# Performance work log

Measured on AMD Instinct MI355X. Metric: run time of the kernel, lower is better.

Reference implementation:

```python
import jax, jax.numpy as jnp
import numpy as np

B, T, H, LAT, ADIM = 8192, 40, 100, 10, 2
ATT_TEMP = 5.0


def setup_inputs() -> dict:
    key = jax.random.key(0)
    ks = jax.random.split(key, 12)
    return {
        "sampled_att_z": jax.random.normal(ks[0], (B, LAT), jnp.float32),
        "enc_h": jax.random.normal(ks[1], (B, H), jnp.float32),
        # keep IDM params strictly positive / physically plausible to avoid inf
        "idm_params": 1.0 + 2.0 * jax.random.uniform(ks[2], (B, 5), jnp.float32),
        "idm_s": jax.random.uniform(ks[3], (B, T, 8), jnp.float32),
        "sdv_acts": jax.random.normal(ks[4], (B, T, ADIM), jnp.float32),
        "linear_W": jax.random.normal(ks[5], (LAT, H), jnp.float32) / np.float32(np.sqrt(LAT)),
        "linear_b": jnp.zeros((H,), jnp.float32),
        "lstm_Wx": jax.random.normal(ks[6], (H + ADIM, 4 * H), jnp.float32) / np.float32(np.sqrt(H + ADIM)),
        "lstm_Wh": jax.random.normal(ks[7], (H, 4 * H), jnp.float32) / np.float32(np.sqrt(H)),
        "lstm_b": jnp.zeros((4 * H,), jnp.float32),
        "att_W": jax.random.normal(ks[8], (H, 1), jnp.float32) / np.float32(np.sqrt(H)),
        "att_b": jnp.zeros((1,), jnp.float32),
        # precomputed per-step noise, replacing tf.random.normal inside the loop
        "noise_f": jax.random.normal(ks[9], (T, B, 1), jnp.float32),
        "noise_m": jax.random.normal(ks[10], (T, B, 1), jnp.float32),
    }


def reference(sampled_att_z, enc_h, idm_params, idm_s, sdv_acts,
              linear_W, linear_b, lstm_Wx, lstm_Wh, lstm_b, att_W, att_b,
              noise_f, noise_m):
    desired_v = idm_params[:, 0:1]
    desired_tgap = idm_params[:, 1:2]
    min_jamx = idm_params[:, 2:3]
    max_act = idm_params[:, 3:4]
    min_act = idm_params[:, 4:5]

    def idm_driver(vel, dv, dx):  # all [B,1]
        dx = jnp.clip(dx, 0.5, 1000.0)
        desired_gap = min_jamx + jax.nn.relu(
            desired_tgap * vel + vel * dv / (2.0 * jnp.sqrt(max_act * min_act)))
        act = max_act * (1.0 - (vel / desired_v) ** 4 - (desired_gap / dx) ** 2)
        return jnp.clip(act, -3.0, 3.0)

    att_proj = sampled_att_z @ linear_W + linear_b  # [B,H]; also the att_context and init h,c

    s_tm = jnp.swapaxes(idm_s, 0, 1)      # [T,B,8]
    a_tm = jnp.swapaxes(sdv_acts, 0, 1)   # [T,B,ADIM]

    ego_v0 = idm_s[:, 0, 0:1]
    ego_x0 = idm_s[:, 0, 3:4]
    zero_act = jnp.zeros_like(ego_v0)  # step-0 kinematic update is a no-op

    def step(carry, xs):
        ego_v, ego_x, h, c, act = carry
        s, sdv, nf, nm = xs
        ego_v = ego_v + act * 0.1
        ego_x = ego_x + ego_v * 0.1 + 0.5 * act * 0.1 ** 2

        f_v, m_v = s[:, 1:2], s[:, 2:3]
        f_x, m_x = s[:, 4:5], s[:, 5:6]
        f_ex, m_ex = s[:, 6:7], s[:, 7:8]

        ef_act = idm_driver(ego_v, ego_v - f_v, f_x - ego_x)
        ef_act = f_ex * ef_act + (1.0 - f_ex) * nf
        em_act = idm_driver(ego_v, ego_v - m_v, m_x - ego_x)
        em_act = m_ex * em_act + (1.0 - m_ex) * nm

        x_in = jnp.concatenate([att_proj, sdv], axis=-1)  # [B,H+ADIM]
        z = x_in @ lstm_Wx + h @ lstm_Wh + lstm_b          # [B,4H], keras gate order i,f,g,o
        zi, zf, zg, zo = jnp.split(z, 4, axis=-1)
        c = jax.nn.sigmoid(zf) * c + jax.nn.sigmoid(zi) * jnp.tanh(zg)
        h = jax.nn.sigmoid(zo) * jnp.tanh(c)

        att_score = jax.nn.sigmoid(ATT_TEMP * (h @ att_W + att_b))  # [B,1]
        act = (1.0 - att_score) * ef_act + att_score * em_act
        return (ego_v, ego_x, h, c, act), (act, att_score)

    init = (ego_v0, ego_x0, att_proj, att_proj, zero_act)
    _, (acts, atts) = jax.lax.scan(step, init, (s_tm, a_tm, noise_f, noise_m))
    act_seq = jnp.swapaxes(acts, 0, 1)  # [B,T,1]
    att_seq = jnp.swapaxes(atts, 0, 1)  # [B,T,1]
    return act_seq, att_seq
```

## Files before the change

### kernel.cpp

```cpp
#include <hip/hip_runtime.h>
#include <math.h>


#define B_TOT 8192
#define T_STEPS 40
#define NB 16

typedef _Float16 f16;
typedef f16 f16x8 __attribute__((ext_vector_type(8)));
typedef float f32x4 __attribute__((ext_vector_type(4)));

__device__ __forceinline__ float rcpf(float x) { return __builtin_amdgcn_rcpf(x); }
__device__ __forceinline__ float ex2(float x)  { return __builtin_amdgcn_exp2f(x); }
__device__ __forceinline__ float sigf(float x)  { return rcpf(1.f + ex2(-1.44269504f * x)); }
__device__ __forceinline__ float tanhf_(float x){ return fmaf(-2.f, rcpf(1.f + ex2(2.88539008f * x)), 1.f); }


__global__ __launch_bounds__(256) void idm_prep(
    const float* __restrict__ Wx, const float* __restrict__ Wh,
    const float* __restrict__ bvec, const float* __restrict__ attw,
    f16* __restrict__ whb, f16* __restrict__ wxb,
    float* __restrict__ bp)
{
  int i = blockIdx.x * 256 + threadIdx.x;
  int k = i >> 9, n = i & 511;
  int g = n >> 7, j128 = n & 127;
  float vh = 0.f, vx = 0.f;
  if (j128 < 100) {
    int col = g * 100 + j128;
    if (k < 100)      { vh = Wh[k * 400 + col]; vx = Wx[k * 400 + col]; }
    else if (k < 102) { vh = Wx[k * 400 + col]; }
  } else if (n == 100 && k < 100) {
    vh = attw[k];
  }
  int idx = (((n >> 4) * 4 + (k >> 5)) * 64 + (((k >> 3) & 3) * 16 + (n & 15))) * 8 + (k & 7);
  whb[idx] = (f16)vh;
  wxb[idx] = (f16)vx;
  if (i < 512) { int gg = i >> 7, jj = i & 127; bp[i] = (jj < 100) ? bvec[gg * 100 + jj] : 0.f; }
}

__global__ __launch_bounds__(448, 4) void idm_main(
    const float* __restrict__ z_att,
    const float* __restrict__ linear_W,
    const float* __restrict__ linear_b,
    const float* __restrict__ sdv_acts,
    const f16* __restrict__ whb, const f16* __restrict__ wxb,
    const float* __restrict__ bp,
    const float* __restrict__ idm_params,
    const float* __restrict__ idm_s,
    const float* __restrict__ att_b,
    const float* __restrict__ noise_f,
    const float* __restrict__ noise_m,
    float* __restrict__ out)
{
  __shared__ f16   hS[2][16][136];
  __shared__ f16   sdvS[T_STEPS][16][2];
  __shared__ float logitS[T_STEPS][16];
  __shared__ float sS[16][T_STEPS][6];
  __shared__ float nS[2][T_STEPS][16];
  __shared__ float accS[2][16][T_STEPS];

  const int tid = threadIdx.x;
  const int w  = tid >> 6;
  const int l  = tid & 63;
  const int lr = l & 15;
  const int lq = l >> 4;
  const int b0g = blockIdx.x * NB;
  const int jcol = 16 * w + lr;

  for (int idx = tid; idx < 2176; idx += 448) ((unsigned*)hS)[idx] = 0u;
  for (int idx = tid; idx < 1280; idx += 448) {
    float v = sdv_acts[(size_t)b0g * 80 + idx];
    int b = idx / 80, r = idx - b * 80;
    sdvS[r >> 1][b][r & 1] = (f16)v;
  }
  for (int idx = tid; idx < 5120; idx += 448) {
    int f = idx & 7;
    if (f != 0 && f != 3) {
      int b = idx / 320, rem = idx - b * 320, t = rem >> 3;
      sS[b][t][(f < 3) ? f - 1 : f - 2] = idm_s[(size_t)b0g * 320 + idx];
    }
  }
  for (int idx = tid; idx < 1280; idx += 448) {
    int which = idx >= 640 ? 1 : 0;
    int r = idx - which * 640;
    int t = r >> 4, i = r & 15;
    nS[which][t][i] = which ? noise_m[(size_t)t * B_TOT + b0g + i]
                            : noise_f[(size_t)t * B_TOT + b0g + i];
  }
  __syncthreads();

  if (tid < 256) {
    int b = tid >> 4, oct = tid & 15;
    float za[10];
    #pragma unroll
    for (int t2 = 0; t2 < 10; ++t2) za[t2] = z_att[(b0g + b) * 10 + t2];
    #pragma unroll
    for (int jj = 0; jj < 8; ++jj) {
      int j = oct * 8 + jj;
      if (j < 100) {
        float acc = linear_b[j];
        #pragma unroll
        for (int t2 = 0; t2 < 10; ++t2) acc = fmaf(za[t2], linear_W[t2 * 100 + j], acc);
        hS[0][b][j] = (f16)acc;
      }
    }
  }
  if (tid < 32) hS[0][tid >> 1][100 + (tid & 1)] = sdvS[0][tid >> 1][tid & 1];
  __syncthreads();

  f16x8 wb[4][4];
  #pragma unroll
  for (int g = 0; g < 4; ++g) {
    int tile = w + 8 * g;
    #pragma unroll
    for (int kf = 0; kf < 4; ++kf)
      wb[g][kf] = *(const f16x8*)(wxb + ((size_t)(tile * 4 + kf) * 64 + l) * 8);
  }
  f32x4 cx[4];
  #pragma unroll
  for (int g = 0; g < 4; ++g) {
    float bpv = bp[(w + 8 * g) * 16 + lr];
    f32x4 c = {bpv, bpv, bpv, bpv};
    cx[g] = c;
  }
  #pragma unroll
  for (int kf = 0; kf < 4; ++kf) {
    f16x8 a = *(const f16x8*)(&hS[0][lr][kf * 32 + lq * 8]);
    #pragma unroll
    for (int g = 0; g < 4; ++g)
      cx[g] = __builtin_amdgcn_mfma_f32_16x16x32_f16(a, wb[g][kf], cx[g], 0, 0, 0);
  }
  #pragma unroll
  for (int g = 0; g < 4; ++g) {
    int tile = w + 8 * g;
    #pragma unroll
    for (int kf = 0; kf < 4; ++kf)
      wb[g][kf] = *(const f16x8*)(whb + ((size_t)(tile * 4 + kf) * 64 + l) * 8);
  }

  float cst[4];
  #pragma unroll
  for (int r = 0; r < 4; ++r) cst[r] = (float)hS[0][lq * 4 + r][jcol];

  int p = 0;
  for (int t = 0; t < T_STEPS; ++t) {
    f16x8 a0 = *(const f16x8*)(&hS[p][lr][0  + lq * 8]);
    f16x8 a1 = *(const f16x8*)(&hS[p][lr][32 + lq * 8]);
    f16x8 a2 = *(const f16x8*)(&hS[p][lr][64 + lq * 8]);
    f16x8 a3 = *(const f16x8*)(&hS[p][lr][96 + lq * 8]);
    f32x4 z0 = cx[0], z1 = cx[1], z2 = cx[2], z3 = cx[3];
    z0 = __builtin_amdgcn_mfma_f32_16x16x32_f16(a0, wb[0][0], z0, 0, 0, 0);
    z1 = __builtin_amdgcn_mfma_f32_16x16x32_f16(a0, wb[1][0], z1, 0, 0, 0);
    z2 = __builtin_amdgcn_mfma_f32_16x16x32_f16(a0, wb[2][0], z2, 0, 0, 0);
    z3 = __builtin_amdgcn_mfma_f32_16x16x32_f16(a0, wb[3][0], z3, 0, 0, 0);
    z0 = __builtin_amdgcn_mfma_f32_16x16x32_f16(a1, wb[0][1], z0, 0, 0, 0);
    z1 = __builtin_amdgcn_mfma_f32_16x16x32_f16(a1, wb[1][1], z1, 0, 0, 0);
    z2 = __builtin_amdgcn_mfma_f32_16x16x32_f16(a1, wb[2][1], z2, 0, 0, 0);
    z3 = __builtin_amdgcn_mfma_f32_16x16x32_f16(a1, wb[3][1], z3, 0, 0, 0);
    z0 = __builtin_amdgcn_mfma_f32_16x16x32_f16(a2, wb[0][2], z0, 0, 0, 0);
    z1 = __builtin_amdgcn_mfma_f32_16x16x32_f16(a2, wb[1][2], z1, 0, 0, 0);
    z2 = __builtin_amdgcn_mfma_f32_16x16x32_f16(a2, wb[2][2], z2, 0, 0, 0);
    z3 = __builtin_amdgcn_mfma_f32_16x16x32_f16(a2, wb[3][2], z3, 0, 0, 0);
    z0 = __builtin_amdgcn_mfma_f32_16x16x32_f16(a3, wb[0][3], z0, 0, 0, 0);
    z1 = __builtin_amdgcn_mfma_f32_16x16x32_f16(a3, wb[1][3], z1, 0, 0, 0);
    z2 = __builtin_amdgcn_mfma_f32_16x16x32_f16(a3, wb[2][3], z2, 0, 0, 0);
    z3 = __builtin_amdgcn_mfma_f32_16x16x32_f16(a3, wb[3][3], z3, 0, 0, 0);

    if (w == 6 && t > 0 && lr == 4) {
      #pragma unroll
      for (int r = 0; r < 4; ++r) logitS[t - 1][lq * 4 + r] = z0[r];
    }

    #pragma unroll
    for (int r = 0; r < 4; ++r) {
      float si = sigf(z0[r]);
      float sf = sigf(z1[r]);
      float tg = tanhf_(z2[r]);
      float so = sigf(z3[r]);
      float cc = fmaf(sf, cst[r], si * tg);
      float hh = so * tanhf_(cc);
      cst[r] = cc;
      if (jcol < 100) hS[p ^ 1][lq * 4 + r][jcol] = (f16)hh;
    }
    if (t + 1 < T_STEPS && tid < 32)
      hS[p ^ 1][tid >> 1][100 + (tid & 1)] = sdvS[t + 1][tid >> 1][tid & 1];
    __syncthreads();
    p ^= 1;
  }

  if (w == 6) {
    f32x4 zL = {0.f, 0.f, 0.f, 0.f};
    #pragma unroll
    for (int kf = 0; kf < 4; ++kf) {
      f16x8 a = *(const f16x8*)(&hS[p][lr][kf * 32 + lq * 8]);
      zL = __builtin_amdgcn_mfma_f32_16x16x32_f16(a, wb[0][kf], zL, 0, 0, 0);
    }
    if (lr == 4) {
      #pragma unroll
      for (int r = 0; r < 4; ++r) logitS[T_STEPS - 1][lq * 4 + r] = zL[r];
    }
  }
  __syncthreads();

  if (tid < 16) {
    int b = b0g + tid;
    const float* P = idm_params + (size_t)b * 5;
    float des_v = P[0], des_tg = P[1], min_jx = P[2], max_a = P[3];
    float inv2s = 0.5f / sqrtf(max_a * P[4]);
    float inv_dv = rcpf(des_v);
    float ego_v = idm_s[(size_t)b * 320 + 0];
    float ego_x = idm_s[(size_t)b * 320 + 3];
    float attb = att_b[0];
    float act = 0.f;
    #pragma unroll 4
    for (int t = 0; t < T_STEPS; ++t) {
      float2 s01 = *(const float2*)&sS[tid][t][0];
      float2 s23 = *(const float2*)&sS[tid][t][2];
      float2 s45 = *(const float2*)&sS[tid][t][4];
      float nf = nS[0][t][tid], nm = nS[1][t][tid];
      float lg = attb + logitS[t][tid];
      ego_v += act * 0.1f;
      ego_x += ego_v * 0.1f + act * 0.005f;
      float af_, am_;
      {
        float dx = fminf(fmaxf(s23.x - ego_x, 0.5f), 1000.f);
        float dg = min_jx + fmaxf(0.f, des_tg * ego_v + ego_v * (ego_v - s01.x) * inv2s);
        float r = ego_v * inv_dv; float r2 = r * r; float q = dg * rcpf(dx);
        af_ = fminf(fmaxf(max_a * (1.f - r2 * r2 - q * q), -3.f), 3.f);
      }
      {
        float dx = fminf(fmaxf(s23.y - ego_x, 0.5f), 1000.f);
        float dg = min_jx + fmaxf(0.f, des_tg * ego_v + ego_v * (ego_v - s01.y) * inv2s);
        float r = ego_v * inv_dv; float r2 = r * r; float q = dg * rcpf(dx);
        am_ = fminf(fmaxf(max_a * (1.f - r2 * r2 - q * q), -3.f), 3.f);
      }
      float ef2 = s45.x * af_ + (1.f - s45.x) * nf;
      float em2 = s45.y * am_ + (1.f - s45.y) * nm;
      float att = sigf(5.f * lg);
      act = (1.f - att) * ef2 + att * em2;
      accS[0][tid][t] = act;
      accS[1][tid][t] = att;
    }
  }
  __syncthreads();

  if (tid < 160) {
    f32x4 va = ((const f32x4*)&accS[0][0][0])[tid];
    f32x4 vt = ((const f32x4*)&accS[1][0][0])[tid];
    *(f32x4*)(out + (size_t)b0g * T_STEPS + tid * 4) = va;
    *(f32x4*)(out + (size_t)B_TOT * T_STEPS + (size_t)b0g * T_STEPS + tid * 4) = vt;
  }
}

extern "C" void kernel_launch(void* const* d_in, const int* in_sizes, int n_in,
                              void* d_out, int out_size, void* d_ws, size_t ws_size,
                              hipStream_t stream) {
  const float* z_att      = (const float*)d_in[0];
  const float* idm_params = (const float*)d_in[2];
  const float* idm_s      = (const float*)d_in[3];
  const float* sdv_acts   = (const float*)d_in[4];
  const float* linear_W   = (const float*)d_in[5];
  const float* linear_b   = (const float*)d_in[6];
  const float* lstm_Wx    = (const float*)d_in[7];
  const float* lstm_Wh    = (const float*)d_in[8];
  const float* lstm_b     = (const float*)d_in[9];
  const float* att_W      = (const float*)d_in[10];
  const float* att_b      = (const float*)d_in[11];
  const float* noise_f    = (const float*)d_in[12];
  const float* noise_m    = (const float*)d_in[13];
  float* out = (float*)d_out;

  f16*   whb = (f16*)d_ws;
  f16*   wxb = (f16*)((char*)d_ws + 131072);
  float* bp  = (float*)((char*)d_ws + 262144);

  idm_prep<<<256, 256, 0, stream>>>(lstm_Wx, lstm_Wh, lstm_b, att_W, whb, wxb, bp);
  idm_main<<<B_TOT / NB, 448, 0, stream>>>(z_att, linear_W, linear_b, sdv_acts,
                                           whb, wxb, bp,
                                           idm_params, idm_s, att_b,
                                           noise_f, noise_m, out);
}
```

Before: 178.9 us.

## Process two 16-row batch tiles per block to amortize weights and barriers

Doubles the batch rows per workgroup from 16 to 32, running two independent MFMA chains (A and B) per warp against the same register-resident weight fragments. This halves the number of blocks and the per-step barrier count per batch row, and gives the MFMA pipe independent work to interleave. In exchange it raises register pressure (launch bounds drop from 4 to 2 blocks per CU), doubles shared memory per block, and serializes twice as many gate activations per step.

```diff
diff --git a/kernel.cpp b/kernel.cpp
--- a/kernel.cpp
+++ b/kernel.cpp
@@ -4,7 +4,7 @@
 
 #define B_TOT 8192
 #define T_STEPS 40
-#define NB 16
+#define NB 32
 
 typedef _Float16 f16;
 typedef f16 f16x8 __attribute__((ext_vector_type(8)));
@@ -39,7 +39,9 @@
   if (i < 512) { int gg = i >> 7, jj = i & 127; bp[i] = (jj < 100) ? bvec[gg * 100 + jj] : 0.f; }
 }
 
-__global__ __launch_bounds__(448, 4) void idm_main(
+#define MM(z, a, g, kf) z = __builtin_amdgcn_mfma_f32_16x16x32_f16(a, wb[g][kf], z, 0, 0, 0)
+
+__global__ __launch_bounds__(448, 2) void idm_main(
     const float* __restrict__ z_att,
     const float* __restrict__ linear_W,
     const float* __restrict__ linear_b,
@@ -53,12 +55,12 @@
     const float* __restrict__ noise_m,
     float* __restrict__ out)
 {
-  __shared__ f16   hS[2][16][136];
-  __shared__ f16   sdvS[T_STEPS][16][2];
-  __shared__ float logitS[T_STEPS][16];
-  __shared__ float sS[16][T_STEPS][6];
-  __shared__ float nS[2][T_STEPS][16];
-  __shared__ float accS[2][16][T_STEPS];
+  __shared__ f16   hS[2][2][16][136];
+  __shared__ f16   sdvS[T_STEPS][32][2];
+  __shared__ float logitS[T_STEPS][32];
+  __shared__ float sS[32][T_STEPS][6];
+  __shared__ float nS[2][T_STEPS][32];
+  __shared__ float accS[2][32][T_STEPS];
 
   const int tid = threadIdx.x;
   const int w  = tid >> 6;
@@ -68,33 +70,33 @@
   const int b0g = blockIdx.x * NB;
   const int jcol = 16 * w + lr;
 
-  for (int idx = tid; idx < 2176; idx += 448) ((unsigned*)hS)[idx] = 0u;
-  for (int idx = tid; idx < 1280; idx += 448) {
+  for (int idx = tid; idx < 4352; idx += 448) ((unsigned*)hS)[idx] = 0u;
+  for (int idx = tid; idx < 2560; idx += 448) {
     float v = sdv_acts[(size_t)b0g * 80 + idx];
     int b = idx / 80, r = idx - b * 80;
     sdvS[r >> 1][b][r & 1] = (f16)v;
   }
-  for (int idx = tid; idx < 5120; idx += 448) {
+  for (int idx = tid; idx < 10240; idx += 448) {
     int f = idx & 7;
     if (f != 0 && f != 3) {
       int b = idx / 320, rem = idx - b * 320, t = rem >> 3;
       sS[b][t][(f < 3) ? f - 1 : f - 2] = idm_s[(size_t)b0g * 320 + idx];
     }
   }
-  for (int idx = tid; idx < 1280; idx += 448) {
-    int which = idx >= 640 ? 1 : 0;
-    int r = idx - which * 640;
-    int t = r >> 4, i = r & 15;
+  for (int idx = tid; idx < 2560; idx += 448) {
+    int which = idx >= 1280 ? 1 : 0;
+    int r = idx - which * 1280;
+    int t = r >> 5, i = r & 31;
     nS[which][t][i] = which ? noise_m[(size_t)t * B_TOT + b0g + i]
                             : noise_f[(size_t)t * B_TOT + b0g + i];
   }
   __syncthreads();
 
-  if (tid < 256) {
-    int b = tid >> 4, oct = tid & 15;
+  for (int s = tid; s < 512; s += 448) {
+    int lb = s >> 4, oct = s & 15;
     float za[10];
     #pragma unroll
-    for (int t2 = 0; t2 < 10; ++t2) za[t2] = z_att[(b0g + b) * 10 + t2];
+    for (int t2 = 0; t2 < 10; ++t2) za[t2] = z_att[(size_t)(b0g + lb) * 10 + t2];
     #pragma unroll
     for (int jj = 0; jj < 8; ++jj) {
       int j = oct * 8 + jj;
@@ -102,11 +104,11 @@
         float acc = linear_b[j];
         #pragma unroll
         for (int t2 = 0; t2 < 10; ++t2) acc = fmaf(za[t2], linear_W[t2 * 100 + j], acc);
-        hS[0][b][j] = (f16)acc;
-      }
-    }
-  }
-  if (tid < 32) hS[0][tid >> 1][100 + (tid & 1)] = sdvS[0][tid >> 1][tid & 1];
+        hS[lb >> 4][0][lb & 15][j] = (f16)acc;
+      }
+    }
+  }
+  if (tid < 64) hS[tid >> 5][0][(tid >> 1) & 15][100 + (tid & 1)] = sdvS[0][tid >> 1][tid & 1];
   __syncthreads();
 
   f16x8 wb[4][4];
@@ -117,19 +119,22 @@
     for (int kf = 0; kf < 4; ++kf)
       wb[g][kf] = *(const f16x8*)(wxb + ((size_t)(tile * 4 + kf) * 64 + l) * 8);
   }
-  f32x4 cx[4];
+  f32x4 cxA[4], cxB[4];
   #pragma unroll
   for (int g = 0; g < 4; ++g) {
     float bpv = bp[(w + 8 * g) * 16 + lr];
     f32x4 c = {bpv, bpv, bpv, bpv};
-    cx[g] = c;
+    cxA[g] = c; cxB[g] = c;
   }
   #pragma unroll
   for (int kf = 0; kf < 4; ++kf) {
-    f16x8 a = *(const f16x8*)(&hS[0][lr][kf * 32 + lq * 8]);
-    #pragma unroll
-    for (int g = 0; g < 4; ++g)
-      cx[g] = __builtin_amdgcn_mfma_f32_16x16x32_f16(a, wb[g][kf], cx[g], 0, 0, 0);
+    f16x8 aA = *(const f16x8*)(&hS[0][0][lr][kf * 32 + lq * 8]);
+    f16x8 aB = *(const f16x8*)(&hS[1][0][lr][kf * 32 + lq * 8]);
+    #pragma unroll
+    for (int g = 0; g < 4; ++g) {
+      cxA[g] = __builtin_amdgcn_mfma_f32_16x16x32_f16(aA, wb[g][kf], cxA[g], 0, 0, 0);
+      cxB[g] = __builtin_amdgcn_mfma_f32_16x16x32_f16(aB, wb[g][kf], cxB[g], 0, 0, 0);
+    }
   }
   #pragma unroll
   for (int g = 0; g < 4; ++g) {
@@ -139,72 +144,92 @@
       wb[g][kf] = *(const f16x8*)(whb + ((size_t)(tile * 4 + kf) * 64 + l) * 8);
   }
 
-  float cst[4];
-  #pragma unroll
-  for (int r = 0; r < 4; ++r) cst[r] = (float)hS[0][lq * 4 + r][jcol];
+  float cstA[4], cstB[4];
+  #pragma unroll
+  for (int r = 0; r < 4; ++r) {
+    cstA[r] = (float)hS[0][0][lq * 4 + r][jcol];
+    cstB[r] = (float)hS[1][0][lq * 4 + r][jcol];
+  }
 
   int p = 0;
   for (int t = 0; t < T_STEPS; ++t) {
-    f16x8 a0 = *(const f16x8*)(&hS[p][lr][0  + lq * 8]);
-    f16x8 a1 = *(const f16x8*)(&hS[p][lr][32 + lq * 8]);
-    f16x8 a2 = *(const f16x8*)(&hS[p][lr][64 + lq * 8]);
-    f16x8 a3 = *(const f16x8*)(&hS[p][lr][96 + lq * 8]);
-    f32x4 z0 = cx[0], z1 = cx[1], z2 = cx[2], z3 = cx[3];
-    z0 = __builtin_amdgcn_mfma_f32_16x16x32_f16(a0, wb[0][0], z0, 0, 0, 0);
-    z1 = __builtin_amdgcn_mfma_f32_16x16x32_f16(a0, wb[1][0], z1, 0, 0, 0);
-    z2 = __builtin_amdgcn_mfma_f32_16x16x32_f16(a0, wb[2][0], z2, 0, 0, 0);
-    z3 = __builtin_amdgcn_mfma_f32_16x16x32_f16(a0, wb[3][0], z3, 0, 0, 0);
-    z0 = __builtin_amdgcn_mfma_f32_16x16x32_f16(a1, wb[0][1], z0, 0, 0, 0);
-    z1 = __builtin_amdgcn_mfma_f32_16x16x32_f16(a1, wb[1][1], z1, 0, 0, 0);
-    z2 = __builtin_amdgcn_mfma_f32_16x16x32_f16(a1, wb[2][1], z2, 0, 0, 0);
-    z3 = __builtin_amdgcn_mfma_f32_16x16x32_f16(a1, wb[3][1], z3, 0, 0, 0);
-    z0 = __builtin_amdgcn_mfma_f32_16x16x32_f16(a2, wb[0][2], z0, 0, 0, 0);
-    z1 = __builtin_amdgcn_mfma_f32_16x16x32_f16(a2, wb[1][2], z1, 0, 0, 0);
-    z2 = __builtin_amdgcn_mfma_f32_16x16x32_f16(a2, wb[2][2], z2, 0, 0, 0);
-    z3 = __builtin_amdgcn_mfma_f32_16x16x32_f16(a2, wb[3][2], z3, 0, 0, 0);
-    z0 = __builtin_amdgcn_mfma_f32_16x16x32_f16(a3, wb[0][3], z0, 0, 0, 0);
-    z1 = __builtin_amdgcn_mfma_f32_16x16x32_f16(a3, wb[1][3], z1, 0, 0, 0);
-    z2 = __builtin_amdgcn_mfma_f32_16x16x32_f16(a3, wb[2][3], z2, 0, 0, 0);
-    z3 = __builtin_amdgcn_mfma_f32_16x16x32_f16(a3, wb[3][3], z3, 0, 0, 0);
+    f16x8 aA0 = *(const f16x8*)(&hS[0][p][lr][0  + lq * 8]);
+    f16x8 aA1 = *(const f16x8*)(&hS[0][p][lr][32 + lq * 8]);
+    f16x8 aA2 = *(const f16x8*)(&hS[0][p][lr][64 + lq * 8]);
+    f16x8 aA3 = *(const f16x8*)(&hS[0][p][lr][96 + lq * 8]);
+    f16x8 aB0 = *(const f16x8*)(&hS[1][p][lr][0  + lq * 8]);
+    f16x8 aB1 = *(const f16x8*)(&hS[1][p][lr][32 + lq * 8]);
+    f16x8 aB2 = *(const f16x8*)(&hS[1][p][lr][64 + lq * 8]);
+    f16x8 aB3 = *(const f16x8*)(&hS[1][p][lr][96 + lq * 8]);
+    f32x4 zA0 = cxA[0], zA1 = cxA[1], zA2 = cxA[2], zA3 = cxA[3];
+    f32x4 zB0 = cxB[0], zB1 = cxB[1], zB2 = cxB[2], zB3 = cxB[3];
+    MM(zA0,aA0,0,0); MM(zA1,aA0,1,0); MM(zA2,aA0,2,0); MM(zA3,aA0,3,0);
+    MM(zA0,aA1,0,1); MM(zA1,aA1,1,1); MM(zA2,aA1,2,1); MM(zA3,aA1,3,1);
+    MM(zA0,aA2,0,2); MM(zA1,aA2,1,2); MM(zA2,aA2,2,2); MM(zA3,aA2,3,2);
+    MM(zA0,aA3,0,3); MM(zA1,aA3,1,3); MM(zA2,aA3,2,3); MM(zA3,aA3,3,3);
+    MM(zB0,aB0,0,0); MM(zB1,aB0,1,0); MM(zB2,aB0,2,0); MM(zB3,aB0,3,0);
+    MM(zB0,aB1,0,1); MM(zB1,aB1,1,1); MM(zB2,aB1,2,1); MM(zB3,aB1,3,1);
+    MM(zB0,aB2,0,2); MM(zB1,aB2,1,2); MM(zB2,aB2,2,2); MM(zB3,aB2,3,2);
+    MM(zB0,aB3,0,3); MM(zB1,aB3,1,3); MM(zB2,aB3,2,3); MM(zB3,aB3,3,3);
 
     if (w == 6 && t > 0 && lr == 4) {
       #pragma unroll
-      for (int r = 0; r < 4; ++r) logitS[t - 1][lq * 4 + r] = z0[r];
+      for (int r = 0; r < 4; ++r) {
+        logitS[t - 1][lq * 4 + r]      = zA0[r];
+        logitS[t - 1][16 + lq * 4 + r] = zB0[r];
+      }
     }
 
     #pragma unroll
     for (int r = 0; r < 4; ++r) {
-      float si = sigf(z0[r]);
-      float sf = sigf(z1[r]);
-      float tg = tanhf_(z2[r]);
-      float so = sigf(z3[r]);
-      float cc = fmaf(sf, cst[r], si * tg);
+      float si = sigf(zA0[r]);
+      float sf = sigf(zA1[r]);
+      float tg = tanhf_(zA2[r]);
+      float so = sigf(zA3[r]);
+      float cc = fmaf(sf, cstA[r], si * tg);
       float hh = so * tanhf_(cc);
-      cst[r] = cc;
-      if (jcol < 100) hS[p ^ 1][lq * 4 + r][jcol] = (f16)hh;
-    }
-    if (t + 1 < T_STEPS && tid < 32)
-      hS[p ^ 1][tid >> 1][100 + (tid & 1)] = sdvS[t + 1][tid >> 1][tid & 1];
+      cstA[r] = cc;
+      if (jcol < 100) hS[0][p ^ 1][lq * 4 + r][jcol] = (f16)hh;
+    }
+    #pragma unroll
+    for (int r = 0; r < 4; ++r) {
+      float si = sigf(zB0[r]);
+      float sf = sigf(zB1[r]);
+      float tg = tanhf_(zB2[r]);
+      float so = sigf(zB3[r]);
+      float cc = fmaf(sf, cstB[r], si * tg);
+      float hh = so * tanhf_(cc);
+      cstB[r] = cc;
+      if (jcol < 100) hS[1][p ^ 1][lq * 4 + r][jcol] = (f16)hh;
+    }
+    if (t + 1 < T_STEPS && tid < 64)
+      hS[tid >> 5][p ^ 1][(tid >> 1) & 15][100 + (tid & 1)] = sdvS[t + 1][tid >> 1][tid & 1];
     __syncthreads();
     p ^= 1;
   }
 
   if (w == 6) {
-    f32x4 zL = {0.f, 0.f, 0.f, 0.f};
+    f32x4 zLA = {0.f, 0.f, 0.f, 0.f}, zLB = {0.f, 0.f, 0.f, 0.f};
     #pragma unroll
     for (int kf = 0; kf < 4; ++kf) {
-      f16x8 a = *(const f16x8*)(&hS[p][lr][kf * 32 + lq * 8]);
-      zL = __builtin_amdgcn_mfma_f32_16x16x32_f16(a, wb[0][kf], zL, 0, 0, 0);
+      f16x8 aA = *(const f16x8*)(&hS[0][p][lr][kf * 32 + lq * 8]);
+      f16x8 aB = *(const f16x8*)(&hS[1][p][lr][kf * 32 + lq * 8]);
+      zLA = __builtin_amdgcn_mfma_f32_16x16x32_f16(aA, wb[0][kf], zLA, 0, 0, 0);
+      zLB = __builtin_amdgcn_mfma_f32_16x16x32_f16(aB, wb[0][kf], zLB, 0, 0, 0);
     }
     if (lr == 4) {
       #pragma unroll
-      for (int r = 0; r < 4; ++r) logitS[T_STEPS - 1][lq * 4 + r] = zL[r];
+      for (int r = 0; r < 4; ++r) {
+        logitS[T_STEPS - 1][lq * 4 + r]      = zLA[r];
+        logitS[T_STEPS - 1][16 + lq * 4 + r] = zLB[r];
+      }
     }
   }
   __syncthreads();
 
-  if (tid < 16) {
-    int b = b0g + tid;
+  if (tid < 32) {
+    int lb = tid;
+    int b = b0g + lb;
     const float* P = idm_params + (size_t)b * 5;
     float des_v = P[0], des_tg = P[1], min_jx = P[2], max_a = P[3];
     float inv2s = 0.5f / sqrtf(max_a * P[4]);
@@ -215,11 +240,11 @@
     float act = 0.f;
     #pragma unroll 4
     for (int t = 0; t < T_STEPS; ++t) {
-      float2 s01 = *(const float2*)&sS[tid][t][0];
-      float2 s23 = *(const float2*)&sS[tid][t][2];
-      float2 s45 = *(const float2*)&sS[tid][t][4];
-      float nf = nS[0][t][tid], nm = nS[1][t][tid];
-      float lg = attb + logitS[t][tid];
+      float2 s01 = *(const float2*)&sS[lb][t][0];
+      float2 s23 = *(const float2*)&sS[lb][t][2];
+      float2 s45 = *(const float2*)&sS[lb][t][4];
+      float nf = nS[0][t][lb], nm = nS[1][t][lb];
+      float lg = attb + logitS[t][lb];
       ego_v += act * 0.1f;
       ego_x += ego_v * 0.1f + act * 0.005f;
       float af_, am_;
@@ -239,13 +264,13 @@
       float em2 = s45.y * am_ + (1.f - s45.y) * nm;
       float att = sigf(5.f * lg);
       act = (1.f - att) * ef2 + att * em2;
-      accS[0][tid][t] = act;
-      accS[1][tid][t] = att;
+      accS[0][lb][t] = act;
+      accS[1][lb][t] = att;
     }
   }
   __syncthreads();
 
-  if (tid < 160) {
+  if (tid < 320) {
     f32x4 va = ((const f32x4*)&accS[0][0][0])[tid];
     f32x4 vt = ((const f32x4*)&accS[1][0][0])[tid];
     *(f32x4*)(out + (size_t)b0g * T_STEPS + tid * 4) = va;
```

Result: slower. 189.1 us (+5.7%).

## Overlap the serial IDM tail with the LSTM recurrence using a dedicated eighth wave

Applied to the files above, without the earlier changes.

Adds an eighth wavefront (512 threads per block) that runs the per-batch IDM driver and attention-mixing step two timesteps behind the LSTM waves, inside the same loop. It also takes over copying the sdv inputs into the h buffer. The aim is to hide the 40-step serial tail that previously ran on 16 threads after the recurrence finished. In exchange the block grows by one wave, which may reduce occupancy, and every timestep's barrier now also waits on the tail work.

```diff
diff --git a/kernel.cpp b/kernel.cpp
--- a/kernel.cpp
+++ b/kernel.cpp
@@ -39,7 +39,9 @@
   if (i < 512) { int gg = i >> 7, jj = i & 127; bp[i] = (jj < 100) ? bvec[gg * 100 + jj] : 0.f; }
 }
 
-__global__ __launch_bounds__(448, 4) void idm_main(
+#define MM(z, a, g, kf) z = __builtin_amdgcn_mfma_f32_16x16x32_f16(a, wb[g][kf], z, 0, 0, 0)
+
+__global__ __launch_bounds__(512, 4) void idm_main(
     const float* __restrict__ z_att,
     const float* __restrict__ linear_W,
     const float* __restrict__ linear_b,
@@ -68,20 +70,20 @@
   const int b0g = blockIdx.x * NB;
   const int jcol = 16 * w + lr;
 
-  for (int idx = tid; idx < 2176; idx += 448) ((unsigned*)hS)[idx] = 0u;
-  for (int idx = tid; idx < 1280; idx += 448) {
+  for (int idx = tid; idx < 2176; idx += 512) ((unsigned*)hS)[idx] = 0u;
+  for (int idx = tid; idx < 1280; idx += 512) {
     float v = sdv_acts[(size_t)b0g * 80 + idx];
     int b = idx / 80, r = idx - b * 80;
     sdvS[r >> 1][b][r & 1] = (f16)v;
   }
-  for (int idx = tid; idx < 5120; idx += 448) {
+  for (int idx = tid; idx < 5120; idx += 512) {
     int f = idx & 7;
     if (f != 0 && f != 3) {
       int b = idx / 320, rem = idx - b * 320, t = rem >> 3;
       sS[b][t][(f < 3) ? f - 1 : f - 2] = idm_s[(size_t)b0g * 320 + idx];
     }
   }
-  for (int idx = tid; idx < 1280; idx += 448) {
+  for (int idx = tid; idx < 1280; idx += 512) {
     int which = idx >= 640 ? 1 : 0;
     int r = idx - which * 640;
     int t = r >> 4, i = r & 15;
@@ -110,81 +112,117 @@
   __syncthreads();
 
   f16x8 wb[4][4];
-  #pragma unroll
-  for (int g = 0; g < 4; ++g) {
-    int tile = w + 8 * g;
-    #pragma unroll
-    for (int kf = 0; kf < 4; ++kf)
-      wb[g][kf] = *(const f16x8*)(wxb + ((size_t)(tile * 4 + kf) * 64 + l) * 8);
-  }
   f32x4 cx[4];
-  #pragma unroll
-  for (int g = 0; g < 4; ++g) {
-    float bpv = bp[(w + 8 * g) * 16 + lr];
-    f32x4 c = {bpv, bpv, bpv, bpv};
-    cx[g] = c;
-  }
-  #pragma unroll
-  for (int kf = 0; kf < 4; ++kf) {
-    f16x8 a = *(const f16x8*)(&hS[0][lr][kf * 32 + lq * 8]);
-    #pragma unroll
-    for (int g = 0; g < 4; ++g)
-      cx[g] = __builtin_amdgcn_mfma_f32_16x16x32_f16(a, wb[g][kf], cx[g], 0, 0, 0);
-  }
-  #pragma unroll
-  for (int g = 0; g < 4; ++g) {
-    int tile = w + 8 * g;
-    #pragma unroll
-    for (int kf = 0; kf < 4; ++kf)
-      wb[g][kf] = *(const f16x8*)(whb + ((size_t)(tile * 4 + kf) * 64 + l) * 8);
-  }
-
   float cst[4];
-  #pragma unroll
-  for (int r = 0; r < 4; ++r) cst[r] = (float)hS[0][lq * 4 + r][jcol];
+  if (w < 7) {
+    #pragma unroll
+    for (int g = 0; g < 4; ++g) {
+      int tile = w + 8 * g;
+      #pragma unroll
+      for (int kf = 0; kf < 4; ++kf)
+        wb[g][kf] = *(const f16x8*)(wxb + ((size_t)(tile * 4 + kf) * 64 + l) * 8);
+    }
+    #pragma unroll
+    for (int g = 0; g < 4; ++g) {
+      float bpv = bp[(w + 8 * g) * 16 + lr];
+      f32x4 c = {bpv, bpv, bpv, bpv};
+      cx[g] = c;
+    }
+    #pragma unroll
+    for (int kf = 0; kf < 4; ++kf) {
+      f16x8 a = *(const f16x8*)(&hS[0][lr][kf * 32 + lq * 8]);
+      #pragma unroll
+      for (int g = 0; g < 4; ++g)
+        cx[g] = __builtin_amdgcn_mfma_f32_16x16x32_f16(a, wb[g][kf], cx[g], 0, 0, 0);
+    }
+    #pragma unroll
+    for (int g = 0; g < 4; ++g) {
+      int tile = w + 8 * g;
+      #pragma unroll
+      for (int kf = 0; kf < 4; ++kf)
+        wb[g][kf] = *(const f16x8*)(whb + ((size_t)(tile * 4 + kf) * 64 + l) * 8);
+    }
+    #pragma unroll
+    for (int r = 0; r < 4; ++r) cst[r] = (float)hS[0][lq * 4 + r][jcol];
+  }
+
+  float des_v = 0.f, des_tg = 0.f, min_jx = 0.f, max_a = 0.f;
+  float inv2s = 0.f, inv_dv = 0.f, ego_v = 0.f, ego_x = 0.f, attb = 0.f, actT = 0.f;
+  if (w == 7 && l < NB) {
+    int b = b0g + l;
+    const float* P = idm_params + (size_t)b * 5;
+    des_v = P[0]; des_tg = P[1]; min_jx = P[2]; max_a = P[3];
+    inv2s = 0.5f / sqrtf(max_a * P[4]);
+    inv_dv = rcpf(des_v);
+    ego_v = idm_s[(size_t)b * 320 + 0];
+    ego_x = idm_s[(size_t)b * 320 + 3];
+    attb = att_b[0];
+    actT = 0.f;
+  }
+
+  auto tail_step = [&](int tt) {
+    float2 s01 = *(const float2*)&sS[l][tt][0];
+    float2 s23 = *(const float2*)&sS[l][tt][2];
+    float2 s45 = *(const float2*)&sS[l][tt][4];
+    float nf = nS[0][tt][l], nm = nS[1][tt][l];
+    float lg = attb + logitS[tt][l];
+    ego_v += actT * 0.1f;
+    ego_x += ego_v * 0.1f + actT * 0.005f;
+    float af_, am_;
+    {
+      float dx = fminf(fmaxf(s23.x - ego_x, 0.5f), 1000.f);
+      float dg = min_jx + fmaxf(0.f, des_tg * ego_v + ego_v * (ego_v - s01.x) * inv2s);
+      float r = ego_v * inv_dv; float r2 = r * r; float q = dg * rcpf(dx);
+      af_ = fminf(fmaxf(max_a * (1.f - r2 * r2 - q * q), -3.f), 3.f);
+    }
+    {
+      float dx = fminf(fmaxf(s23.y - ego_x, 0.5f), 1000.f);
+      float dg = min_jx + fmaxf(0.f, des_tg * ego_v + ego_v * (ego_v - s01.y) * inv2s);
+      float r = ego_v * inv_dv; float r2 = r * r; float q = dg * rcpf(dx);
+      am_ = fminf(fmaxf(max_a * (1.f - r2 * r2 - q * q), -3.f), 3.f);
+    }
+    float ef2 = s45.x * af_ + (1.f - s45.x) * nf;
+    float em2 = s45.y * am_ + (1.f - s45.y) * nm;
+    float att = sigf(5.f * lg);
+    actT = (1.f - att) * ef2 + att * em2;
+    accS[0][l][tt] = actT;
+    accS[1][l][tt] = att;
+  };
 
   int p = 0;
   for (int t = 0; t < T_STEPS; ++t) {
-    f16x8 a0 = *(const f16x8*)(&hS[p][lr][0  + lq * 8]);
-    f16x8 a1 = *(const f16x8*)(&hS[p][lr][32 + lq * 8]);
-    f16x8 a2 = *(const f16x8*)(&hS[p][lr][64 + lq * 8]);
-    f16x8 a3 = *(const f16x8*)(&hS[p][lr][96 + lq * 8]);
-    f32x4 z0 = cx[0], z1 = cx[1], z2 = cx[2], z3 = cx[3];
-    z0 = __builtin_amdgcn_mfma_f32_16x16x32_f16(a0, wb[0][0], z0, 0, 0, 0);
-    z1 = __builtin_amdgcn_mfma_f32_16x16x32_f16(a0, wb[1][0], z1, 0, 0, 0);
-    z2 = __builtin_amdgcn_mfma_f32_16x16x32_f16(a0, wb[2][0], z2, 0, 0, 0);
-    z3 = __builtin_amdgcn_mfma_f32_16x16x32_f16(a0, wb[3][0], z3, 0, 0, 0);
-    z0 = __builtin_amdgcn_mfma_f32_16x16x32_f16(a1, wb[0][1], z0, 0, 0, 0);
-    z1 = __builtin_amdgcn_mfma_f32_16x16x32_f16(a1, wb[1][1], z1, 0, 0, 0);
-    z2 = __builtin_amdgcn_mfma_f32_16x16x32_f16(a1, wb[2][1], z2, 0, 0, 0);
-    z3 = __builtin_amdgcn_mfma_f32_16x16x32_f16(a1, wb[3][1], z3, 0, 0, 0);
-    z0 = __builtin_amdgcn_mfma_f32_16x16x32_f16(a2, wb[0][2], z0, 0, 0, 0);
-    z1 = __builtin_amdgcn_mfma_f32_16x16x32_f16(a2, wb[1][2], z1, 0, 0, 0);
-    z2 = __builtin_amdgcn_mfma_f32_16x16x32_f16(a2, wb[2][2], z2, 0, 0, 0);
-    z3 = __builtin_amdgcn_mfma_f32_16x16x32_f16(a2, wb[3][2], z3, 0, 0, 0);
-    z0 = __builtin_amdgcn_mfma_f32_16x16x32_f16(a3, wb[0][3], z0, 0, 0, 0);
-    z1 = __builtin_amdgcn_mfma_f32_16x16x32_f16(a3, wb[1][3], z1, 0, 0, 0);
-    z2 = __builtin_amdgcn_mfma_f32_16x16x32_f16(a3, wb[2][3], z2, 0, 0, 0);
-    z3 = __builtin_amdgcn_mfma_f32_16x16x32_f16(a3, wb[3][3], z3, 0, 0, 0);
-
-    if (w == 6 && t > 0 && lr == 4) {
-      #pragma unroll
-      for (int r = 0; r < 4; ++r) logitS[t - 1][lq * 4 + r] = z0[r];
-    }
-
-    #pragma unroll
-    for (int r = 0; r < 4; ++r) {
-      float si = sigf(z0[r]);
-      float sf = sigf(z1[r]);
-      float tg = tanhf_(z2[r]);
-      float so = sigf(z3[r]);
-      float cc = fmaf(sf, cst[r], si * tg);
-      float hh = so * tanhf_(cc);
-      cst[r] = cc;
-      if (jcol < 100) hS[p ^ 1][lq * 4 + r][jcol] = (f16)hh;
-    }
-    if (t + 1 < T_STEPS && tid < 32)
-      hS[p ^ 1][tid >> 1][100 + (tid & 1)] = sdvS[t + 1][tid >> 1][tid & 1];
+    if (w < 7) {
+      f16x8 a0 = *(const f16x8*)(&hS[p][lr][0  + lq * 8]);
+      f16x8 a1 = *(const f16x8*)(&hS[p][lr][32 + lq * 8]);
+      f16x8 a2 = *(const f16x8*)(&hS[p][lr][64 + lq * 8]);
+      f16x8 a3 = *(const f16x8*)(&hS[p][lr][96 + lq * 8]);
+      f32x4 z0 = cx[0], z1 = cx[1], z2 = cx[2], z3 = cx[3];
+      MM(z0,a0,0,0); MM(z1,a0,1,0); MM(z2,a0,2,0); MM(z3,a0,3,0);
+      MM(z0,a1,0,1); MM(z1,a1,1,1); MM(z2,a1,2,1); MM(z3,a1,3,1);
+      MM(z0,a2,0,2); MM(z1,a2,1,2); MM(z2,a2,2,2); MM(z3,a2,3,2);
+      MM(z0,a3,0,3); MM(z1,a3,1,3); MM(z2,a3,2,3); MM(z3,a3,3,3);
+
+      if (w == 6 && t > 0 && lr == 4) {
+        #pragma unroll
+        for (int r = 0; r < 4; ++r) logitS[t - 1][lq * 4 + r] = z0[r];
+      }
+
+      #pragma unroll
+      for (int r = 0; r < 4; ++r) {
+        float si = sigf(z0[r]);
+        float sf = sigf(z1[r]);
+        float tg = tanhf_(z2[r]);
+        float so = sigf(z3[r]);
+        float cc = fmaf(sf, cst[r], si * tg);
+        float hh = so * tanhf_(cc);
+        cst[r] = cc;
+        if (jcol < 100) hS[p ^ 1][lq * 4 + r][jcol] = (f16)hh;
+      }
+    } else {
+      if (t + 1 < T_STEPS && l < 32)
+        hS[p ^ 1][l >> 1][100 + (l & 1)] = sdvS[t + 1][l >> 1][l & 1];
+      if (t >= 2 && l < NB) tail_step(t - 2);
+    }
     __syncthreads();
     p ^= 1;
   }
@@ -201,48 +239,9 @@
       for (int r = 0; r < 4; ++r) logitS[T_STEPS - 1][lq * 4 + r] = zL[r];
     }
   }
-  __syncthreads();
-
-  if (tid < 16) {
-    int b = b0g + tid;
-    const float* P = idm_params + (size_t)b * 5;
-    float des_v = P[0], des_tg = P[1], min_jx = P[2], max_a = P[3];
-    float inv2s = 0.5f / sqrtf(max_a * P[4]);
-    float inv_dv = rcpf(des_v);
-    float ego_v = idm_s[(size_t)b * 320 + 0];
-    float ego_x = idm_s[(size_t)b * 320 + 3];
-    float attb = att_b[0];
-    float act = 0.f;
-    #pragma unroll 4
-    for (int t = 0; t < T_STEPS; ++t) {
-      float2 s01 = *(const float2*)&sS[tid][t][0];
-      float2 s23 = *(const float2*)&sS[tid][t][2];
-      float2 s45 = *(const float2*)&sS[tid][t][4];
-      float nf = nS[0][t][tid], nm = nS[1][t][tid];
-      float lg = attb + logitS[t][tid];
-      ego_v += act * 0.1f;
-      ego_x += ego_v * 0.1f + act * 0.005f;
-      float af_, am_;
-      {
-        float dx = fminf(fmaxf(s23.x - ego_x, 0.5f), 1000.f);
-        float dg = min_jx + fmaxf(0.f, des_tg * ego_v + ego_v * (ego_v - s01.x) * inv2s);
-        float r = ego_v * inv_dv; float r2 = r * r; float q = dg * rcpf(dx);
-        af_ = fminf(fmaxf(max_a * (1.f - r2 * r2 - q * q), -3.f), 3.f);
-      }
-      {
-        float dx = fminf(fmaxf(s23.y - ego_x, 0.5f), 1000.f);
-        float dg = min_jx + fmaxf(0.f, des_tg * ego_v + ego_v * (ego_v - s01.y) * inv2s);
-        float r = ego_v * inv_dv; float r2 = r * r; float q = dg * rcpf(dx);
-        am_ = fminf(fmaxf(max_a * (1.f - r2 * r2 - q * q), -3.f), 3.f);
-      }
-      float ef2 = s45.x * af_ + (1.f - s45.x) * nf;
-      float em2 = s45.y * am_ + (1.f - s45.y) * nm;
-      float att = sigf(5.f * lg);
-      act = (1.f - att) * ef2 + att * em2;
-      accS[0][tid][t] = act;
-      accS[1][tid][t] = att;
-    }
-  }
+  if (w == 7 && l < NB) tail_step(T_STEPS - 2);
+  __syncthreads();
+  if (w == 7 && l < NB) tail_step(T_STEPS - 1);
   __syncthreads();
 
   if (tid < 160) {
@@ -276,7 +275,7 @@
   float* bp  = (float*)((char*)d_ws + 262144);
 
   idm_prep<<<256, 256, 0, stream>>>(lstm_Wx, lstm_Wh, lstm_b, att_W, whb, wxb, bp);
-  idm_main<<<B_TOT / NB, 448, 0, stream>>>(z_att, linear_W, linear_b, sdv_acts,
+  idm_main<<<B_TOT / NB, 512, 0, stream>>>(z_att, linear_W, linear_b, sdv_acts,
                                            whb, wxb, bp,
                                            idm_params, idm_s, att_b,
                                            noise_f, noise_m, out);
```

Measured after the change: 180.3 us. About the same (+0.8%).
